# Kernel optimization log

Measured on AMD Instinct MI355X. Metric: run time of the kernel, lower is better.

## Reference

```python
import jax, jax.numpy as jnp
import numpy as np

B, N, D, Kp = 32, 4096, 128, 256  # batch*heads, seq_len, head_dim, linformer proj dim


def setup_inputs() -> dict:
    key = jax.random.key(0)
    ks = jax.random.split(key, 7)
    return {
        "Q": jax.random.normal(ks[0], (B, N, D), dtype=jnp.float32),
        "K": jax.random.normal(ks[1], (B, N, D), dtype=jnp.float32),
        "V": jax.random.normal(ks[2], (B, N, D), dtype=jnp.float32),
        "E_W": jax.random.normal(ks[3], (Kp, N), dtype=jnp.float32) * (1.0 / np.sqrt(N)),
        "E_b": jax.random.normal(ks[4], (Kp,), dtype=jnp.float32) * 0.02,
        "F_W": jax.random.normal(ks[5], (Kp, N), dtype=jnp.float32) * (1.0 / np.sqrt(N)),
        "F_b": jax.random.normal(ks[6], (Kp,), dtype=jnp.float32) * 0.02,
    }


def reference(Q, K, V, E_W, E_b, F_W, F_b):
    d = Q.shape[-1]
    scale = 1.0 / jnp.sqrt(jnp.asarray(d, Q.dtype))
    # E projection on K^T: [B,d,n] @ W^T -> [B,d,k]
    K_proj = jnp.einsum('bnd,kn->bdk', K, E_W) + E_b  # bias broadcasts over k axis
    # scaled scores [B,n,k], softmax over projected dim k
    scores = jnp.einsum('bnd,bdk->bnk', Q, K_proj) * scale
    P_bar = jax.nn.softmax(scores, axis=-1)
    # F projection on V^T then transpose back: [B,k,d]
    V_proj = jnp.einsum('bnd,kn->bkd', V, F_W) + F_b[:, None]
    # [B,n,k] @ [B,k,d] -> [B,n,d]
    return jnp.einsum('bnk,bkd->bnd', P_bar, V_proj)
```

## Files before the change

kernel.cpp:

```cpp
#include <hip/hip_runtime.h>
#include <cstdint>
#include <cstddef>

#define N_SEQ 4096
#define D_HEAD 128
#define KP_DIM 256

typedef __attribute__((ext_vector_type(4))) float f32x4;
typedef __attribute__((ext_vector_type(8))) short bf16x8;
typedef __attribute__((ext_vector_type(2))) unsigned int u32x2;

static __device__ __forceinline__ short f2bf(float f) {
  uint32_t u = __builtin_bit_cast(uint32_t, f);
  u += 0x7FFFu + ((u >> 16) & 1u);
  return (short)(u >> 16);
}

static __device__ __forceinline__ float bf2f(short h) {
  return __builtin_bit_cast(float, (uint32_t)((uint16_t)h) << 16);
}

static __device__ __forceinline__ unsigned int cvtpk(float a, float b) {
  unsigned int r;
  asm("v_cvt_pk_bf16_f32 %0, %1, %2" : "=v"(r) : "v"(a), "v"(b));
  return r;
}

static __device__ __forceinline__ int swz8(int r) { return (r ^ (r >> 2)) & 7; }

__global__ __launch_bounds__(256) void conv_w_kernel(
    const float* __restrict__ EW, const float* __restrict__ FW,
    short* __restrict__ wbf) {
  const int idx = blockIdx.x * 256 + threadIdx.x;
  const int half = 262144;
  f32x4 v = (idx < half) ? *(const f32x4*)(EW + (size_t)idx * 4)
                         : *(const f32x4*)(FW + (size_t)(idx - half) * 4);
  u32x2 h = {cvtpk(v[0], v[1]), cvtpk(v[2], v[3])};
  *(u32x2*)(wbf + (size_t)idx * 4) = h;
}

__global__ __launch_bounds__(1024, 4) void proj_partial_kernel(
    const float* __restrict__ Kin, const float* __restrict__ Vin,
    const short* __restrict__ wbf, short* __restrict__ pws) {
  const int bid = blockIdx.x;
  const int wk = (bid & 7) * 32 + (bid >> 3);
  const int b = wk & 31;
  const int s = (wk >> 5) & 3;
  const int p = wk >> 7;

  const float* __restrict__ X = (p == 0 ? Kin : Vin) + (size_t)b * (N_SEQ * D_HEAD);
  const short* __restrict__ wp = wbf + (size_t)p * (KP_DIM * N_SEQ);
  short* __restrict__ outp = pws + ((((size_t)b * 2 + p) * 4) + s) * (KP_DIM * D_HEAD);

  __shared__ __align__(16) short lw[2][KP_DIM * 64];
  __shared__ __align__(16) short xt[2][D_HEAD * 64];

  const int t = threadIdx.x;
  const int lane = t & 63;
  const int w = t >> 6;
  const int wkk = (w >> 1) * 32;
  const int wdd = (w & 1) * 64;
  const int l15 = lane & 15;
  const int l4 = lane >> 4;
  const int dq = t & 31;
  const int ng = t >> 5;

  const int n0 = s * 1024;

  f32x4 acc[2][4];
#pragma unroll
  for (int i = 0; i < 2; ++i)
#pragma unroll
    for (int j = 0; j < 4; ++j) acc[i][j] = (f32x4){0.f, 0.f, 0.f, 0.f};

  f32x4 xA[2], xB[2];

#define PROJ_WISSUE(BUF, NC)                                                        \
  do {                                                                              \
    _Pragma("unroll") for (int i_ = 0; i_ < 2; ++i_) {                              \
      int g_ = t + i_ * 1024;                                                       \
      int row_ = g_ >> 3, c_ = g_ & 7;                                              \
      __builtin_amdgcn_global_load_lds(                                             \
          (const __attribute__((address_space(1))) void*)(wp + (size_t)row_ * N_SEQ \
              + (NC) + ((c_ ^ swz8(row_)) << 3)),                                   \
          (__attribute__((address_space(3))) void*)(&lw[BUF][g_ * 8]), 16, 0, 0);   \
    }                                                                               \
  } while (0)

#define PROJ_XISSUE(XR, NC)                                                         \
  do {                                                                              \
    _Pragma("unroll") for (int i_ = 0; i_ < 2; ++i_)                                \
      XR[i_] = *(const f32x4*)(X + (size_t)((NC) + ng * 2 + i_) * D_HEAD + dq * 4); \
  } while (0)

#define PROJ_XCVT(XR, BUF)                                                          \
  do {                                                                              \
    _Pragma("unroll") for (int j_ = 0; j_ < 4; ++j_) {                              \
      int drow_ = dq * 4 + j_;                                                      \
      unsigned int hv_ = cvtpk(XR[0][j_], XR[1][j_]);                               \
      *(unsigned int*)(&xt[BUF][drow_ * 64 + ((ng * 2) ^ (swz8(drow_) << 3))]) = hv_; \
    }                                                                               \
  } while (0)

#define PROJ_COMPUTE(CUR)                                                           \
  do {                                                                              \
    _Pragma("unroll") for (int ks2 = 0; ks2 < 2; ++ks2) {                           \
      const int col0 = ks2 * 32 + l4 * 8;                                           \
      bf16x8 a_[2], bb_[4];                                                         \
      _Pragma("unroll") for (int mt_ = 0; mt_ < 2; ++mt_) {                         \
        int row_ = wkk + mt_ * 16 + l15;                                            \
        a_[mt_] = *(const bf16x8*)(&lw[CUR][row_ * 64 + (col0 ^ (swz8(row_) << 3))]); \
      }                                                                             \
      _Pragma("unroll") for (int nt_ = 0; nt_ < 4; ++nt_) {                         \
        int row_ = wdd + nt_ * 16 + l15;                                            \
        bb_[nt_] = *(const bf16x8*)(&xt[CUR][row_ * 64 + (col0 ^ (swz8(row_) << 3))]); \
      }                                                                             \
      _Pragma("unroll") for (int mt_ = 0; mt_ < 2; ++mt_)                           \
        _Pragma("unroll") for (int nt_ = 0; nt_ < 4; ++nt_)                         \
          acc[mt_][nt_] = __builtin_amdgcn_mfma_f32_16x16x32_bf16(a_[mt_], bb_[nt_], \
                                                                  acc[mt_][nt_], 0, 0, 0); \
    }                                                                               \
  } while (0)

  PROJ_XISSUE(xA, n0);
  PROJ_WISSUE(0, n0);
  asm volatile("s_waitcnt vmcnt(2)" ::: "memory");
  PROJ_XCVT(xA, 0);
  PROJ_XISSUE(xB, n0 + 64);
  asm volatile("s_waitcnt vmcnt(2)" ::: "memory");
  __syncthreads();

  for (int itp = 0; itp < 7; ++itp) {
    const int it0 = itp * 2;
    PROJ_WISSUE(1, n0 + (it0 + 1) * 64);
    PROJ_XISSUE(xA, n0 + (it0 + 2) * 64);
    asm volatile("s_waitcnt vmcnt(4)" ::: "memory");
    PROJ_XCVT(xB, 1);
    PROJ_COMPUTE(0);
    asm volatile("s_waitcnt vmcnt(2)" ::: "memory");
    __syncthreads();
    PROJ_WISSUE(0, n0 + (it0 + 2) * 64);
    PROJ_XISSUE(xB, n0 + (it0 + 3) * 64);
    asm volatile("s_waitcnt vmcnt(4)" ::: "memory");
    PROJ_XCVT(xA, 0);
    PROJ_COMPUTE(1);
    asm volatile("s_waitcnt vmcnt(2)" ::: "memory");
    __syncthreads();
  }
  PROJ_WISSUE(1, n0 + 15 * 64);
  asm volatile("s_waitcnt vmcnt(2)" ::: "memory");
  PROJ_XCVT(xB, 1);
  PROJ_COMPUTE(0);
  asm volatile("s_waitcnt vmcnt(0)" ::: "memory");
  __syncthreads();
  PROJ_COMPUTE(1);

#undef PROJ_WISSUE
#undef PROJ_XISSUE
#undef PROJ_XCVT
#undef PROJ_COMPUTE

#pragma unroll
  for (int mt = 0; mt < 2; ++mt)
#pragma unroll
    for (int nt = 0; nt < 4; ++nt)
#pragma unroll
      for (int r = 0; r < 4; ++r) {
        int kk = wkk + mt * 16 + l4 * 4 + r;
        int dd = wdd + nt * 16 + l15;
        outp[kk * D_HEAD + dd] = f2bf(acc[mt][nt][r]);
      }
}

__global__ __launch_bounds__(256) void reduce_bias_kernel(
    const short* __restrict__ pws, const float* __restrict__ Eb,
    const float* __restrict__ Fb, short* __restrict__ kp, short* __restrict__ vpt) {
  const int q = blockIdx.x & 7;
  const int b = blockIdx.x >> 3;
  const int t = threadIdx.x;
  __shared__ short tile[64 * 128];
  if (q < 4) {
    const short* __restrict__ base = pws + ((size_t)b * 2) * 4 * 32768;
    const int off = q * 8192;
    for (int i = t; i < 8192; i += 256) {
      int ii = off + i;
      int k = ii >> 7;
      float v = bf2f(base[ii]) + bf2f(base[ii + 32768]) + bf2f(base[ii + 65536]) +
                bf2f(base[ii + 98304]) + Eb[k];
      kp[(size_t)b * 32768 + ii] = f2bf(v);
    }
  } else {
    const int kq = q - 4;
    const short* __restrict__ base =
        pws + (((size_t)b * 2 + 1) * 4) * 32768 + kq * 64 * D_HEAD;
    for (int i = t; i < 8192; i += 256) {
      int kl = i >> 7, d = i & 127;
      float v = bf2f(base[i]) + bf2f(base[i + 32768]) + bf2f(base[i + 65536]) +
                bf2f(base[i + 98304]) + Fb[kq * 64 + kl];
      tile[kl * 128 + (d ^ ((kl & 15) << 3))] = f2bf(v);
    }
    __syncthreads();
    for (int i = t; i < 8192; i += 256) {
      int d = i >> 6, kl = i & 63;
      vpt[(size_t)b * 32768 + d * 256 + kq * 64 + kl] = tile[kl * 128 + (d ^ ((kl & 15) << 3))];
    }
  }
}

__global__ __launch_bounds__(1024, 4) void attn_kernel(
    const float* __restrict__ Q, const short* __restrict__ kp,
    const short* __restrict__ vpt, float* __restrict__ out) {
  const int bid = blockIdx.x;
  const int wk = (bid & 7) * 32 + (bid >> 3);
  const int b = wk >> 3;
  const int slice = wk & 7;
  const int t = threadIdx.x;
  const int lane = t & 63;
  const int w = t >> 6;
  const int l15 = lane & 15, l4 = lane >> 4;

  __shared__ __align__(16) short lbuf[81920];
  short* lkp = lbuf;
  short* lvpt = lbuf + 32768;
  short* lpw = lbuf + 65536 + w * 1024;

  const short* __restrict__ kpb = kp + (size_t)b * 32768;
  const short* __restrict__ vptb = vpt + (size_t)b * 32768;

#pragma unroll
  for (int i = 0; i < 4; ++i) {
    int g = t + i * 1024;
    int row = g >> 4, c = g & 15;
    __builtin_amdgcn_global_load_lds(
        (const __attribute__((address_space(1))) void*)(kpb + (size_t)row * 128 +
                                                        ((c ^ (row & 7)) << 3)),
        (__attribute__((address_space(3))) void*)(&lkp[g * 8]), 16, 0, 0);
  }
#pragma unroll
  for (int i = 0; i < 4; ++i) {
    int g = t + i * 1024;
    int row = g >> 5, c = g & 31;
    __builtin_amdgcn_global_load_lds(
        (const __attribute__((address_space(1))) void*)(vptb + (size_t)row * 256 +
                                                        ((c ^ (row & 7)) << 3)),
        (__attribute__((address_space(3))) void*)(&lvpt[g * 8]), 16, 0, 0);
  }

  const float scale = 0.08838834764831845f;
  f32x4 qraw[8];
  {
    const float* qr = Q + ((size_t)b * N_SEQ + slice * 512 + w * 16 + l15) * D_HEAD;
#pragma unroll
    for (int ks = 0; ks < 4; ++ks) {
      qraw[2 * ks] = *(const f32x4*)(qr + ks * 32 + l4 * 8);
      qraw[2 * ks + 1] = *(const f32x4*)(qr + ks * 32 + l4 * 8 + 4);
    }
  }
  asm volatile("s_waitcnt vmcnt(0)" ::: "memory");
  __syncthreads();

#pragma unroll
  for (int rd = 0; rd < 2; ++rd) {
    const int rowBase = slice * 512 + rd * 256 + w * 16;

    bf16x8 qf[4];
#pragma unroll
    for (int ks = 0; ks < 4; ++ks) {
      union { unsigned int u[4]; bf16x8 v; } cv;
      cv.u[0] = cvtpk(qraw[2 * ks][0] * scale, qraw[2 * ks][1] * scale);
      cv.u[1] = cvtpk(qraw[2 * ks][2] * scale, qraw[2 * ks][3] * scale);
      cv.u[2] = cvtpk(qraw[2 * ks + 1][0] * scale, qraw[2 * ks + 1][1] * scale);
      cv.u[3] = cvtpk(qraw[2 * ks + 1][2] * scale, qraw[2 * ks + 1][3] * scale);
      qf[ks] = cv.v;
    }

    f32x4 accs[16];
#pragma unroll
    for (int i = 0; i < 16; ++i) accs[i] = (f32x4){0.f, 0.f, 0.f, 0.f};
    __builtin_amdgcn_s_setprio(1);
#pragma unroll
    for (int ks = 0; ks < 4; ++ks) {
#pragma unroll
      for (int nt = 0; nt < 16; ++nt) {
        bf16x8 af = *(const bf16x8*)(&lkp[(nt * 16 + l15) * 128 +
                                          (((ks * 4 + l4) ^ (l15 & 7)) << 3)]);
        accs[nt] = __builtin_amdgcn_mfma_f32_16x16x32_bf16(af, qf[ks], accs[nt], 0, 0, 0);
      }
    }
    __builtin_amdgcn_s_setprio(0);

    float m = -1e30f;
#pragma unroll
    for (int nt = 0; nt < 16; ++nt)
#pragma unroll
      for (int r = 0; r < 4; ++r) m = fmaxf(m, accs[nt][r]);
    m = fmaxf(m, __shfl_xor(m, 16));
    m = fmaxf(m, __shfl_xor(m, 32));
    float s = 0.f;
#pragma unroll
    for (int nt = 0; nt < 16; ++nt)
#pragma unroll
      for (int r = 0; r < 4; ++r) {
        float e = __expf(accs[nt][r] - m);
        accs[nt][r] = e;
        s += e;
      }
    s += __shfl_xor(s, 16);
    s += __shfl_xor(s, 32);
    float inv = 1.0f / s;

    f32x4 acco[8];
#pragma unroll
    for (int i = 0; i < 8; ++i) acco[i] = (f32x4){0.f, 0.f, 0.f, 0.f};
#pragma unroll
    for (int qq = 0; qq < 4; ++qq) {
#pragma unroll
      for (int ntl = 0; ntl < 4; ++ntl) {
        int nt = qq * 4 + ntl;
        int cw = 2 * ntl + (l4 >> 1);
        unsigned int p0 = cvtpk(accs[nt][0] * inv, accs[nt][1] * inv);
        unsigned int p1 = cvtpk(accs[nt][2] * inv, accs[nt][3] * inv);
        *(u32x2*)((char*)lpw + l15 * 128 + ((cw ^ (l15 & 7)) << 4) + (l4 & 1) * 8) =
            (u32x2){p0, p1};
      }
      if (rd == 0 && qq == 3) {
        const float* qr = Q + ((size_t)b * N_SEQ + slice * 512 + 256 + w * 16 + l15) * D_HEAD;
#pragma unroll
        for (int ks = 0; ks < 4; ++ks) {
          qraw[2 * ks] = *(const f32x4*)(qr + ks * 32 + l4 * 8);
          qraw[2 * ks + 1] = *(const f32x4*)(qr + ks * 32 + l4 * 8 + 4);
        }
      }
      __builtin_amdgcn_s_setprio(1);
#pragma unroll
      for (int ksl = 0; ksl < 2; ++ksl) {
        bf16x8 pa = *(const bf16x8*)((char*)lpw + l15 * 128 +
                                     (((4 * ksl + l4) ^ (l15 & 7)) << 4));
        int ksa = qq * 2 + ksl;
#pragma unroll
        for (int ntv = 0; ntv < 8; ++ntv) {
          bf16x8 av = *(const bf16x8*)(&lvpt[(ntv * 16 + l15) * 256 +
                                             (((ksa * 4 + l4) ^ (l15 & 7)) << 3)]);
          acco[ntv] = __builtin_amdgcn_mfma_f32_16x16x32_bf16(av, pa, acco[ntv], 0, 0, 0);
        }
      }
      __builtin_amdgcn_s_setprio(0);
    }

    float* ob = out + ((size_t)b * N_SEQ + rowBase) * D_HEAD;
#pragma unroll
    for (int ntv = 0; ntv < 8; ++ntv)
      *(f32x4*)(ob + (size_t)l15 * D_HEAD + ntv * 16 + l4 * 4) = acco[ntv];
  }
}

extern "C" void kernel_launch(void* const* d_in, const int* in_sizes, int n_in,
                              void* d_out, int out_size, void* d_ws, size_t ws_size,
                              hipStream_t stream) {
  const float* Q  = (const float*)d_in[0];
  const float* K  = (const float*)d_in[1];
  const float* V  = (const float*)d_in[2];
  const float* EW = (const float*)d_in[3];
  const float* Eb = (const float*)d_in[4];
  const float* FW = (const float*)d_in[5];
  const float* Fb = (const float*)d_in[6];
  float* out = (float*)d_out;

  short* wbf = (short*)d_out;
  short* pws = (short*)((char*)d_out + 8 * 1024 * 1024);
  short* kpb = (short*)d_ws;
  short* vpt = (short*)((char*)d_ws + (size_t)32 * KP_DIM * D_HEAD * 2);

  conv_w_kernel<<<dim3(2048), dim3(256), 0, stream>>>(EW, FW, wbf);
  proj_partial_kernel<<<dim3(256), dim3(1024), 0, stream>>>(K, V, wbf, pws);
  reduce_bias_kernel<<<dim3(256), dim3(256), 0, stream>>>(pws, Eb, Fb, kpb, vpt);
  attn_kernel<<<dim3(256), dim3(1024), 0, stream>>>(Q, kpb, vpt, out);
}
```

Measured before the change: 85.97 us.

## Split projection into 8 sequence chunks and single-buffer weight LDS

The projection kernel now splits the sequence into 8 chunks of 512 instead of 4 chunks of 1024, launching 512 blocks instead of 256. The weight tile in LDS drops from double to single buffering, which cuts LDS use so more blocks can be resident (launch bounds raised to 8). Compute is moved ahead of the next weight load, with extra barriers added. The reduce kernel now sums 8 bf16 partials instead of 4, which adds partial-workspace traffic and more bf16 rounding. Losing the weight double buffer exposes load latency inside each block.

```diff
diff --git a/kernel.cpp b/kernel.cpp
--- a/kernel.cpp
+++ b/kernel.cpp
@@ -39,20 +39,20 @@
   *(u32x2*)(wbf + (size_t)idx * 4) = h;
 }
 
-__global__ __launch_bounds__(1024, 4) void proj_partial_kernel(
+__global__ __launch_bounds__(1024, 8) void proj_partial_kernel(
     const float* __restrict__ Kin, const float* __restrict__ Vin,
     const short* __restrict__ wbf, short* __restrict__ pws) {
   const int bid = blockIdx.x;
-  const int wk = (bid & 7) * 32 + (bid >> 3);
+  const int wk = (bid & 7) * 64 + (bid >> 3);
+  const int s = wk >> 6;
+  const int p = (wk >> 5) & 1;
   const int b = wk & 31;
-  const int s = (wk >> 5) & 3;
-  const int p = wk >> 7;
 
   const float* __restrict__ X = (p == 0 ? Kin : Vin) + (size_t)b * (N_SEQ * D_HEAD);
   const short* __restrict__ wp = wbf + (size_t)p * (KP_DIM * N_SEQ);
-  short* __restrict__ outp = pws + ((((size_t)b * 2 + p) * 4) + s) * (KP_DIM * D_HEAD);
-
-  __shared__ __align__(16) short lw[2][KP_DIM * 64];
+  short* __restrict__ outp = pws + (((size_t)b * 2 + p) * 8 + s) * (KP_DIM * D_HEAD);
+
+  __shared__ __align__(16) short lw[KP_DIM * 64];
   __shared__ __align__(16) short xt[2][D_HEAD * 64];
 
   const int t = threadIdx.x;
@@ -65,7 +65,7 @@
   const int dq = t & 31;
   const int ng = t >> 5;
 
-  const int n0 = s * 1024;
+  const int n0 = s * 512;
 
   f32x4 acc[2][4];
 #pragma unroll
@@ -75,7 +75,7 @@
 
   f32x4 xA[2], xB[2];
 
-#define PROJ_WISSUE(BUF, NC)                                                        \
+#define PROJ_WISSUE(NC)                                                             \
   do {                                                                              \
     _Pragma("unroll") for (int i_ = 0; i_ < 2; ++i_) {                              \
       int g_ = t + i_ * 1024;                                                       \
@@ -83,7 +83,7 @@
       __builtin_amdgcn_global_load_lds(                                             \
           (const __attribute__((address_space(1))) void*)(wp + (size_t)row_ * N_SEQ \
               + (NC) + ((c_ ^ swz8(row_)) << 3)),                                   \
-          (__attribute__((address_space(3))) void*)(&lw[BUF][g_ * 8]), 16, 0, 0);   \
+          (__attribute__((address_space(3))) void*)(&lw[g_ * 8]), 16, 0, 0);        \
     }                                                                               \
   } while (0)
 
@@ -109,7 +109,7 @@
       bf16x8 a_[2], bb_[4];                                                         \
       _Pragma("unroll") for (int mt_ = 0; mt_ < 2; ++mt_) {                         \
         int row_ = wkk + mt_ * 16 + l15;                                            \
-        a_[mt_] = *(const bf16x8*)(&lw[CUR][row_ * 64 + (col0 ^ (swz8(row_) << 3))]); \
+        a_[mt_] = *(const bf16x8*)(&lw[row_ * 64 + (col0 ^ (swz8(row_) << 3))]);    \
       }                                                                             \
       _Pragma("unroll") for (int nt_ = 0; nt_ < 4; ++nt_) {                         \
         int row_ = wdd + nt_ * 16 + l15;                                            \
@@ -123,34 +123,37 @@
   } while (0)
 
   PROJ_XISSUE(xA, n0);
-  PROJ_WISSUE(0, n0);
+  PROJ_WISSUE(n0);
   asm volatile("s_waitcnt vmcnt(2)" ::: "memory");
   PROJ_XCVT(xA, 0);
   PROJ_XISSUE(xB, n0 + 64);
   asm volatile("s_waitcnt vmcnt(2)" ::: "memory");
   __syncthreads();
 
-  for (int itp = 0; itp < 7; ++itp) {
+  for (int itp = 0; itp < 3; ++itp) {
     const int it0 = itp * 2;
-    PROJ_WISSUE(1, n0 + (it0 + 1) * 64);
+    PROJ_COMPUTE(0);
+    __syncthreads();
+    PROJ_WISSUE(n0 + (it0 + 1) * 64);
     PROJ_XISSUE(xA, n0 + (it0 + 2) * 64);
     asm volatile("s_waitcnt vmcnt(4)" ::: "memory");
     PROJ_XCVT(xB, 1);
-    PROJ_COMPUTE(0);
     asm volatile("s_waitcnt vmcnt(2)" ::: "memory");
     __syncthreads();
-    PROJ_WISSUE(0, n0 + (it0 + 2) * 64);
+    PROJ_COMPUTE(1);
+    __syncthreads();
+    PROJ_WISSUE(n0 + (it0 + 2) * 64);
     PROJ_XISSUE(xB, n0 + (it0 + 3) * 64);
     asm volatile("s_waitcnt vmcnt(4)" ::: "memory");
     PROJ_XCVT(xA, 0);
-    PROJ_COMPUTE(1);
     asm volatile("s_waitcnt vmcnt(2)" ::: "memory");
     __syncthreads();
   }
-  PROJ_WISSUE(1, n0 + 15 * 64);
+  PROJ_COMPUTE(0);
+  __syncthreads();
+  PROJ_WISSUE(n0 + 7 * 64);
   asm volatile("s_waitcnt vmcnt(2)" ::: "memory");
   PROJ_XCVT(xB, 1);
-  PROJ_COMPUTE(0);
   asm volatile("s_waitcnt vmcnt(0)" ::: "memory");
   __syncthreads();
   PROJ_COMPUTE(1);
@@ -180,23 +183,25 @@
   const int t = threadIdx.x;
   __shared__ short tile[64 * 128];
   if (q < 4) {
-    const short* __restrict__ base = pws + ((size_t)b * 2) * 4 * 32768;
+    const short* __restrict__ base = pws + ((size_t)b * 16) * 32768;
     const int off = q * 8192;
     for (int i = t; i < 8192; i += 256) {
       int ii = off + i;
       int k = ii >> 7;
-      float v = bf2f(base[ii]) + bf2f(base[ii + 32768]) + bf2f(base[ii + 65536]) +
-                bf2f(base[ii + 98304]) + Eb[k];
+      float v = Eb[k];
+#pragma unroll
+      for (int m = 0; m < 8; ++m) v += bf2f(base[ii + m * 32768]);
       kp[(size_t)b * 32768 + ii] = f2bf(v);
     }
   } else {
     const int kq = q - 4;
     const short* __restrict__ base =
-        pws + (((size_t)b * 2 + 1) * 4) * 32768 + kq * 64 * D_HEAD;
+        pws + ((size_t)b * 16 + 8) * 32768 + kq * 64 * D_HEAD;
     for (int i = t; i < 8192; i += 256) {
       int kl = i >> 7, d = i & 127;
-      float v = bf2f(base[i]) + bf2f(base[i + 32768]) + bf2f(base[i + 65536]) +
-                bf2f(base[i + 98304]) + Fb[kq * 64 + kl];
+      float v = Fb[kq * 64 + kl];
+#pragma unroll
+      for (int m = 0; m < 8; ++m) v += bf2f(base[i + m * 32768]);
       tile[kl * 128 + (d ^ ((kl & 15) << 3))] = f2bf(v);
     }
     __syncthreads();
@@ -372,7 +377,7 @@
   short* vpt = (short*)((char*)d_ws + (size_t)32 * KP_DIM * D_HEAD * 2);
 
   conv_w_kernel<<<dim3(2048), dim3(256), 0, stream>>>(EW, FW, wbf);
-  proj_partial_kernel<<<dim3(256), dim3(1024), 0, stream>>>(K, V, wbf, pws);
+  proj_partial_kernel<<<dim3(512), dim3(1024), 0, stream>>>(K, V, wbf, pws);
   reduce_bias_kernel<<<dim3(256), dim3(256), 0, stream>>>(pws, Eb, Fb, kpb, vpt);
   attn_kernel<<<dim3(256), dim3(1024), 0, stream>>>(Q, kpb, vpt, out);
 }
```

Result: slower. 162.8 us (+89.4%).
